# Kernel optimization log

Hardware: AMD Instinct MI355X
Metric: run time of the kernel (lower is better)

Reference implementation:

```python
import jax, jax.numpy as jnp
import numpy as np

THETA = 1.2
XI = 0.3


def setup_inputs() -> dict:
    key = jax.random.key(0)
    k1, k2 = jax.random.split(key)
    B, D = 8192, 512
    x = jax.random.normal(k1, (B, D), dtype=jnp.float32)
    y = jax.random.randint(k2, (B,), 0, 1000, dtype=jnp.int64)
    return {"x": x, "y": y}


def reference(x, y):
    B = x.shape[0]
    # per-sample L2 normalization: n_i = x_i / ||x_i||
    n = x / jnp.linalg.norm(x, axis=1, keepdims=True)  # [B, D]
    # pairwise squared distances ||n_i - n_j||^2 = |n_i|^2 + |n_j|^2 - 2 n_i.n_j
    sq = jnp.sum(n * n, axis=1)                        # [B]
    G = n @ n.T                                        # [B, B]
    dist2 = sq[:, None] + sq[None, :] - 2.0 * G        # [B, B]
    # indicator: +1 if same label else -1 (symmetric)
    ind = jnp.where(y[:, None] == y[None, :], 1.0, -1.0)
    # original loops i in [0,B), j in [i,B): upper triangle including diagonal
    idx = jnp.arange(B)
    mask = (idx[None, :] >= idx[:, None]).astype(x.dtype)
    hinge = jnp.maximum(THETA - dist2, 0.0)
    total = jnp.sum(mask * (XI + ind * hinge))
    m_scalar = 1.0 / (B * B - B)
    return m_scalar * total
```

## Files before the change

kernel.cpp:

```cpp
#include <hip/hip_runtime.h>
#include <cstdint>
#include <cstddef>

#define THETA 1.2f
#define XI 0.3f
#define BDIM 8192
#define DDIM 512
#define NTILE 64
#define NUPPER 2080
#define GRID 512
#define NPAIRS_UP (((double)BDIM * (double)(BDIM + 1)) * 0.5)

typedef float f32x4 __attribute__((ext_vector_type(4)));
typedef int i32x8 __attribute__((ext_vector_type(8)));


__global__ __launch_bounds__(256) void normalize_rows(
    const float* __restrict__ x, unsigned char* __restrict__ nf8,
    float* __restrict__ sq, unsigned int* __restrict__ counter)
{
    if (blockIdx.x == 0 && threadIdx.x == 0) { *counter = 0u; }
    int row = blockIdx.x * 4 + (threadIdx.x >> 6);
    int l = threadIdx.x & 63;
    const float4* xr = (const float4*)(x + (size_t)row * DDIM);
    float4 f0 = xr[l];
    float4 f1 = xr[l + 64];
    float s = f0.x*f0.x + f0.y*f0.y + f0.z*f0.z + f0.w*f0.w
            + f1.x*f1.x + f1.y*f1.y + f1.z*f1.z + f1.w*f1.w;
    #pragma unroll
    for (int m = 1; m < 64; m <<= 1) s += __shfl_xor(s, m);
    float rn = rsqrtf(s);
    int pk0 = __builtin_amdgcn_cvt_pk_fp8_f32(f0.x * rn, f0.y * rn, 0, false);
    pk0     = __builtin_amdgcn_cvt_pk_fp8_f32(f0.z * rn, f0.w * rn, pk0, true);
    int pk1 = __builtin_amdgcn_cvt_pk_fp8_f32(f1.x * rn, f1.y * rn, 0, false);
    pk1     = __builtin_amdgcn_cvt_pk_fp8_f32(f1.z * rn, f1.w * rn, pk1, true);
    size_t base = (size_t)(row >> 4) * 4 * 2048;
    int within = ((row & 15) + ((l >> 3) & 3) * 16) * 32 + (l & 7) * 4;
    int kc0 = l >> 5;
    int kc1 = (l >> 5) + 2;
    *(int*)(nf8 + base + (size_t)kc0 * 2048 + within) = pk0;
    *(int*)(nf8 + base + (size_t)kc1 * 2048 + within) = pk1;
    if (l == 0) sq[row] = s * rn * rn;
}

__device__ __forceinline__ void decode_tile(int u, int& ti, int& tj) {
    int t = (int)((sqrtf(8.0f * (float)u + 1.0f) - 1.0f) * 0.5f);
    while ((t + 1) * (t + 2) / 2 <= u) ++t;
    while (t * (t + 1) / 2 > u) --t;
    tj = t;
    ti = u - t * (t + 1) / 2;
}

__global__ __launch_bounds__(512, 4) void gram_hinge(
    const unsigned char* __restrict__ nf8, const float* __restrict__ sq,
    const int* __restrict__ y, double* __restrict__ part,
    unsigned int* __restrict__ counter, float* __restrict__ out)
{
    __shared__ unsigned char As[2][16384];
    __shared__ float wpart[8];
    __shared__ double dpart[8];
    __shared__ int is_last;

    int tid = threadIdx.x;
    int w = tid >> 6, l = tid & 63;
    int wr = w >> 2, wc = w & 3;
    int lr = l & 15, q = l >> 4;

    auto stageA = [&](unsigned char* dAb, int pti, int pc) {
        #pragma unroll
        for (int i = 0; i < 2; ++i) {
            int t = w * 2 + i;
            int rf = t >> 1, half = t & 1;
            const unsigned char* src = nf8
                + ((size_t)((pti * 8 + rf) * 4 + pc)) * 2048 + half * 1024 + l * 16;
            __builtin_amdgcn_global_load_lds(
                (const __attribute__((address_space(1))) void*)src,
                (__attribute__((address_space(3))) void*)(dAb + t * 1024), 16, 0, 0);
        }
    };
    auto bload = [&](int ptj, int pc, i32x8* dst) {
        #pragma unroll
        for (int ni = 0; ni < 2; ++ni)
            dst[ni] = *(const i32x8*)(nf8
                + ((size_t)((ptj * 8 + wc * 2 + ni) * 4 + pc)) * 2048 + l * 32);
    };

    float acc0 = 0.f, acc1 = 0.f;

    int u = blockIdx.x;
    int ti, tj;
    decode_tile(u, ti, tj);

    i32x8 bfe[2], bfo[2];

    bload(tj, 0, bfe);
    stageA(As[0], ti, 0);

    while (u < NUPPER) {
        int u_next = u + GRID;
        bool have_next = (u_next < NUPPER);
        int ti_n = 0, tj_n = 0;
        if (have_next) decode_tile(u_next, ti_n, tj_n);

        f32x4 accv[4][2] = {};

        #pragma unroll 1
        for (int cc = 0; cc < 2; ++cc) {
            bload(tj, 2 * cc + 1, bfo);
            stageA(As[1], ti, 2 * cc + 1);
            asm volatile("s_waitcnt vmcnt(6)" ::: "memory");
            asm volatile("s_barrier" ::: "memory");
            __builtin_amdgcn_s_setprio(1);
            #pragma unroll
            for (int mi = 0; mi < 4; ++mi) {
                i32x8 af = *(const i32x8*)(As[0] + (wr * 4 + mi) * 2048 + l * 32);
                #pragma unroll
                for (int ni = 0; ni < 2; ++ni)
                    accv[mi][ni] = __builtin_amdgcn_mfma_scale_f32_16x16x128_f8f6f4(
                        af, bfe[ni], accv[mi][ni],
                        0, 0, 0, 0x7F7F7F7F, 0, 0x7F7F7F7F);
            }
            __builtin_amdgcn_s_setprio(0);
            asm volatile("s_barrier" ::: "memory");

            bool more = (cc == 0) || have_next;
            int nti = (cc == 0) ? ti : ti_n;
            int ntj = (cc == 0) ? tj : tj_n;
            int nc  = (cc == 0) ? 2 : 0;
            if (more) {
                bload(ntj, nc, bfe);
                stageA(As[0], nti, nc);
                asm volatile("s_waitcnt vmcnt(6)" ::: "memory");
            } else {
                asm volatile("s_waitcnt vmcnt(0)" ::: "memory");
            }
            asm volatile("s_barrier" ::: "memory");
            __builtin_amdgcn_s_setprio(1);
            #pragma unroll
            for (int mi = 0; mi < 4; ++mi) {
                i32x8 af = *(const i32x8*)(As[1] + (wr * 4 + mi) * 2048 + l * 32);
                #pragma unroll
                for (int ni = 0; ni < 2; ++ni)
                    accv[mi][ni] = __builtin_amdgcn_mfma_scale_f32_16x16x128_f8f6f4(
                        af, bfo[ni], accv[mi][ni],
                        0, 0, 0, 0x7F7F7F7F, 0, 0x7F7F7F7F);
            }
            __builtin_amdgcn_s_setprio(0);
            asm volatile("s_barrier" ::: "memory");
        }

        {
            int jb = tj * 128 + wc * 32 + lr;
            float sqj[2]; int yj[2];
            #pragma unroll
            for (int ni = 0; ni < 2; ++ni) {
                sqj[ni] = sq[jb + ni * 16];
                yj[ni]  = y[jb + ni * 16];
            }
            bool skip = (ti == tj) && (wr == 1) && (wc < 2);
            bool full = (ti != tj) || (wc * 32 >= wr * 64 + 64);
            if (!skip) {
                if (full) {
                    #pragma unroll
                    for (int mi = 0; mi < 4; ++mi) {
                        #pragma unroll
                        for (int r = 0; r < 4; ++r) {
                            int ia = ti * 128 + wr * 64 + mi * 16 + q * 4 + r;
                            float ci = THETA - sq[ia];
                            int yi = y[ia];
                            float h0 = fmaxf(fmaf(2.f, accv[mi][0][r], ci - sqj[0]), 0.f);
                            acc0 += (yi == yj[0]) ? h0 : -h0;
                            float h1 = fmaxf(fmaf(2.f, accv[mi][1][r], ci - sqj[1]), 0.f);
                            acc1 += (yi == yj[1]) ? h1 : -h1;
                        }
                    }
                } else {
                    #pragma unroll
                    for (int mi = 0; mi < 4; ++mi) {
                        #pragma unroll
                        for (int r = 0; r < 4; ++r) {
                            int rl_ = wr * 64 + mi * 16 + q * 4 + r;
                            int ia = ti * 128 + rl_;
                            float ci = THETA - sq[ia];
                            int yi = y[ia];
                            #pragma unroll
                            for (int ni = 0; ni < 2; ++ni) {
                                float h = fmaxf(fmaf(2.f, accv[mi][ni][r], ci - sqj[ni]), 0.f);
                                float sh = (yi == yj[ni]) ? h : -h;
                                if (wc * 32 + ni * 16 + lr >= rl_) acc0 += sh;
                            }
                        }
                    }
                }
            }
        }

        u = u_next; ti = ti_n; tj = tj_n;
    }

    float local = acc0 + acc1;
    #pragma unroll
    for (int off = 32; off > 0; off >>= 1) local += __shfl_down(local, off);
    if (l == 0) wpart[w] = local;
    __syncthreads();
    if (tid == 0) {
        double ssum = 0.0;
        #pragma unroll
        for (int i = 0; i < 8; ++i) ssum += (double)wpart[i];
        __hip_atomic_store(&part[blockIdx.x], ssum, __ATOMIC_RELEASE, __HIP_MEMORY_SCOPE_AGENT);
        unsigned int ticket = __hip_atomic_fetch_add(
            counter, 1u, __ATOMIC_ACQ_REL, __HIP_MEMORY_SCOPE_AGENT);
        is_last = (ticket == GRID - 1) ? 1 : 0;
    }
    __syncthreads();
    if (is_last) {
        double s = 0.0;
        for (int i = tid; i < GRID; i += 512)
            s += __hip_atomic_load(&part[i], __ATOMIC_ACQUIRE, __HIP_MEMORY_SCOPE_AGENT);
        #pragma unroll
        for (int off = 32; off > 0; off >>= 1) s += __shfl_down(s, off);
        if (l == 0) dpart[w] = s;
        __syncthreads();
        if (tid == 0) {
            double t8 = 0.0;
            #pragma unroll
            for (int i = 0; i < 8; ++i) t8 += dpart[i];
            double total = t8 + (double)XI * NPAIRS_UP;
            const double m = 1.0 / ((double)BDIM * (double)BDIM - (double)BDIM);
            out[0] = (float)(total * m);
        }
    }
}

extern "C" void kernel_launch(void* const* d_in, const int* in_sizes, int n_in,
                              void* d_out, int out_size, void* d_ws, size_t ws_size,
                              hipStream_t stream) {
    const float* x = (const float*)d_in[0];
    const int* y = (const int*)d_in[1];
    float* out = (float*)d_out;

    unsigned char* nf8 = (unsigned char*)d_ws;
    char* p = (char*)d_ws + (size_t)BDIM * DDIM;
    float* sq = (float*)p;
    unsigned int* counter = (unsigned int*)(p + (size_t)BDIM * 4);
    double* part = (double*)(p + (size_t)BDIM * 4 + 64);

    normalize_rows<<<BDIM / 4, 256, 0, stream>>>(x, nf8, sq, counter);
    gram_hinge<<<GRID, 512, 0, stream>>>(nf8, sq, y, part, counter, out);
}
```

Baseline: 111.6 us.

## Use 256x128 block tiles over triangular row-panel units for higher A reuse

Each work unit now covers a 256-row by 128-column tile, so each wave computes 8x2 MFMA blocks instead of 4x2. The upper triangle is enumerated as 1056 units with a new decode from unit index to panel pair. The A staging buffer in LDS doubles and launch bounds drop to 2 blocks per CU. The aim is to raise arithmetic intensity and reduce B fragment reloads per MFMA, at the cost of fewer units than the 512 blocks (poorer load balance), more diagonal waste and lower occupancy.

```diff
diff --git a/kernel.cpp b/kernel.cpp
--- a/kernel.cpp
+++ b/kernel.cpp
@@ -6,8 +6,9 @@
 #define XI 0.3f
 #define BDIM 8192
 #define DDIM 512
-#define NTILE 64
-#define NUPPER 2080
+#define NROWP 32
+#define NCOLP 64
+#define NUNITS 1056
 #define GRID 512
 #define NPAIRS_UP (((double)BDIM * (double)(BDIM + 1)) * 0.5)
 
@@ -43,20 +44,21 @@
     if (l == 0) sq[row] = s * rn * rn;
 }
 
-__device__ __forceinline__ void decode_tile(int u, int& ti, int& tj) {
-    int t = (int)((sqrtf(8.0f * (float)u + 1.0f) - 1.0f) * 0.5f);
-    while ((t + 1) * (t + 2) / 2 <= u) ++t;
-    while (t * (t + 1) / 2 > u) --t;
-    tj = t;
-    ti = u - t * (t + 1) / 2;
-}
-
-__global__ __launch_bounds__(512, 4) void gram_hinge(
+__device__ __forceinline__ void decode_unit(int u, int& ti, int& tj) {
+    int t = (int)((65.0f - sqrtf(65.0f * 65.0f - 4.0f * (float)u)) * 0.5f);
+    if (t > 31) t = 31;
+    while (t < 31 && (t + 1) * (65 - (t + 1)) <= u) ++t;
+    while (t > 0 && t * (65 - t) > u) --t;
+    ti = t;
+    tj = 2 * t + (u - t * (65 - t));
+}
+
+__global__ __launch_bounds__(512, 2) void gram_hinge(
     const unsigned char* __restrict__ nf8, const float* __restrict__ sq,
     const int* __restrict__ y, double* __restrict__ part,
     unsigned int* __restrict__ counter, float* __restrict__ out)
 {
-    __shared__ unsigned char As[2][16384];
+    __shared__ unsigned char As[2][32768];
     __shared__ float wpart[8];
     __shared__ double dpart[8];
     __shared__ int is_last;
@@ -68,11 +70,11 @@
 
     auto stageA = [&](unsigned char* dAb, int pti, int pc) {
         #pragma unroll
-        for (int i = 0; i < 2; ++i) {
-            int t = w * 2 + i;
+        for (int i = 0; i < 4; ++i) {
+            int t = w * 4 + i;
             int rf = t >> 1, half = t & 1;
             const unsigned char* src = nf8
-                + ((size_t)((pti * 8 + rf) * 4 + pc)) * 2048 + half * 1024 + l * 16;
+                + ((size_t)((pti * 16 + rf) * 4 + pc)) * 2048 + half * 1024 + l * 16;
             __builtin_amdgcn_global_load_lds(
                 (const __attribute__((address_space(1))) void*)src,
                 (__attribute__((address_space(3))) void*)(dAb + t * 1024), 16, 0, 0);
@@ -89,31 +91,31 @@
 
     int u = blockIdx.x;
     int ti, tj;
-    decode_tile(u, ti, tj);
+    decode_unit(u, ti, tj);
 
     i32x8 bfe[2], bfo[2];
 
     bload(tj, 0, bfe);
     stageA(As[0], ti, 0);
 
-    while (u < NUPPER) {
+    while (u < NUNITS) {
         int u_next = u + GRID;
-        bool have_next = (u_next < NUPPER);
+        bool have_next = (u_next < NUNITS);
         int ti_n = 0, tj_n = 0;
-        if (have_next) decode_tile(u_next, ti_n, tj_n);
-
-        f32x4 accv[4][2] = {};
+        if (have_next) decode_unit(u_next, ti_n, tj_n);
+
+        f32x4 accv[8][2] = {};
 
         #pragma unroll 1
         for (int cc = 0; cc < 2; ++cc) {
             bload(tj, 2 * cc + 1, bfo);
             stageA(As[1], ti, 2 * cc + 1);
-            asm volatile("s_waitcnt vmcnt(6)" ::: "memory");
+            asm volatile("s_waitcnt vmcnt(8)" ::: "memory");
             asm volatile("s_barrier" ::: "memory");
             __builtin_amdgcn_s_setprio(1);
             #pragma unroll
-            for (int mi = 0; mi < 4; ++mi) {
-                i32x8 af = *(const i32x8*)(As[0] + (wr * 4 + mi) * 2048 + l * 32);
+            for (int mi = 0; mi < 8; ++mi) {
+                i32x8 af = *(const i32x8*)(As[0] + (wr * 8 + mi) * 2048 + l * 32);
                 #pragma unroll
                 for (int ni = 0; ni < 2; ++ni)
                     accv[mi][ni] = __builtin_amdgcn_mfma_scale_f32_16x16x128_f8f6f4(
@@ -130,15 +132,15 @@
             if (more) {
                 bload(ntj, nc, bfe);
                 stageA(As[0], nti, nc);
-                asm volatile("s_waitcnt vmcnt(6)" ::: "memory");
+                asm volatile("s_waitcnt vmcnt(8)" ::: "memory");
             } else {
                 asm volatile("s_waitcnt vmcnt(0)" ::: "memory");
             }
             asm volatile("s_barrier" ::: "memory");
             __builtin_amdgcn_s_setprio(1);
             #pragma unroll
-            for (int mi = 0; mi < 4; ++mi) {
-                i32x8 af = *(const i32x8*)(As[1] + (wr * 4 + mi) * 2048 + l * 32);
+            for (int mi = 0; mi < 8; ++mi) {
+                i32x8 af = *(const i32x8*)(As[1] + (wr * 8 + mi) * 2048 + l * 32);
                 #pragma unroll
                 for (int ni = 0; ni < 2; ++ni)
                     accv[mi][ni] = __builtin_amdgcn_mfma_scale_f32_16x16x128_f8f6f4(
@@ -157,15 +159,15 @@
                 sqj[ni] = sq[jb + ni * 16];
                 yj[ni]  = y[jb + ni * 16];
             }
-            bool skip = (ti == tj) && (wr == 1) && (wc < 2);
-            bool full = (ti != tj) || (wc * 32 >= wr * 64 + 64);
+            bool skip = (tj == 2 * ti) && (wr == 1);
+            bool full = (tj > 2 * ti + 1) || ((tj == 2 * ti + 1) && (wr == 0));
             if (!skip) {
                 if (full) {
                     #pragma unroll
-                    for (int mi = 0; mi < 4; ++mi) {
+                    for (int mi = 0; mi < 8; ++mi) {
                         #pragma unroll
                         for (int r = 0; r < 4; ++r) {
-                            int ia = ti * 128 + wr * 64 + mi * 16 + q * 4 + r;
+                            int ia = ti * 256 + wr * 128 + mi * 16 + q * 4 + r;
                             float ci = THETA - sq[ia];
                             int yi = y[ia];
                             float h0 = fmaxf(fmaf(2.f, accv[mi][0][r], ci - sqj[0]), 0.f);
@@ -176,11 +178,11 @@
                     }
                 } else {
                     #pragma unroll
-                    for (int mi = 0; mi < 4; ++mi) {
+                    for (int mi = 0; mi < 8; ++mi) {
                         #pragma unroll
                         for (int r = 0; r < 4; ++r) {
-                            int rl_ = wr * 64 + mi * 16 + q * 4 + r;
-                            int ia = ti * 128 + rl_;
+                            int rl_ = mi * 16 + q * 4 + r;
+                            int ia = ti * 256 + wr * 128 + rl_;
                             float ci = THETA - sq[ia];
                             int yi = y[ia];
                             #pragma unroll
```

Measured after the change: 117.3 us. 5.2% more time.
